# Performance work log

Measured on AMD Instinct MI355X. Metric: run time of the kernel, lower is better.

## Reference

```python
import jax, jax.numpy as jnp
import numpy as np

B, T, C, H = 2, 2048, 1024, 16
HD = C // H  # head dim = 64


def setup_inputs() -> dict:
    key = jax.random.key(0)
    ks = jax.random.split(key, 5)
    s = 0.02
    return {
        "x": jax.random.normal(ks[0], (B, T, C), dtype=jnp.float32),
        "w_attn": jax.random.normal(ks[1], (C, 3 * C), dtype=jnp.float32) * s,
        "b_attn": jnp.zeros((3 * C,), dtype=jnp.float32),
        "w_proj": jax.random.normal(ks[2], (C, C), dtype=jnp.float32) * s,
        "b_proj": jnp.zeros((C,), dtype=jnp.float32),
    }


def reference(x, w_attn, b_attn, w_proj, b_proj):
    Bc, Tc, Cc = x.shape
    qkv = x @ w_attn + b_attn                      # [B,T,3C]
    q, k, v = jnp.split(qkv, 3, axis=2)            # each [B,T,C]
    # [B,T,C] -> [B,H,T,HD]
    def heads(t):
        return t.reshape(Bc, Tc, H, HD).transpose(0, 2, 1, 3)
    q, k, v = heads(q), heads(k), heads(v)
    scale = 1.0 / jnp.sqrt(jnp.asarray(HD, dtype=x.dtype))
    att = jnp.einsum("bhqd,bhkd->bhqk", q, k) * scale   # [B,H,T,T]
    causal = jnp.tril(jnp.ones((Tc, Tc), dtype=bool))
    att = jnp.where(causal, att, jnp.asarray(-jnp.inf, dtype=att.dtype))
    att = jax.nn.softmax(att, axis=-1)
    y = jnp.einsum("bhqk,bhkd->bhqd", att, v)            # [B,H,T,HD]
    y = y.transpose(0, 2, 1, 3).reshape(Bc, Tc, Cc)      # [B,T,C]
    return y @ w_proj + b_proj
```

## Files before the change

### kernel.cpp

```cpp
#include <hip/hip_runtime.h>
#include <stdint.h>


typedef short bf16x8 __attribute__((ext_vector_type(8)));
typedef float f32x4 __attribute__((ext_vector_type(4)));

__device__ inline unsigned short f2bf(float f) {
  union { float f; uint32_t u; } v; v.f = f;
  uint32_t u = v.u;
  u += 0x7FFFu + ((u >> 16) & 1u);
  return (unsigned short)(u >> 16);
}

__device__ inline unsigned pkbf(float a, float b) {
  unsigned r;
  asm("v_cvt_pk_bf16_f32 %0, %1, %2" : "=v"(r) : "v"(a), "v"(b));
  return r;
}

__device__ inline float exp2_fast(float x) {
#if __has_builtin(__builtin_amdgcn_exp2f)
  return __builtin_amdgcn_exp2f(x);
#else
  float r; asm("v_exp_f32 %0, %1" : "=v"(r) : "v"(x)); return r;
#endif
}

__device__ inline void load_lds16(const unsigned short* g, unsigned short* l) {
  __builtin_amdgcn_global_load_lds(
      (const __attribute__((address_space(1))) unsigned int*)(const void*)g,
      (__attribute__((address_space(3))) unsigned int*)(void*)l, 16, 0, 0);
}

__global__ __launch_bounds__(256) void cast_bf16_kernel(
    const float* __restrict__ in, unsigned short* __restrict__ out, int n4) {
  int i = blockIdx.x * 256 + threadIdx.x;
  if (i >= n4) return;
  float4 f = reinterpret_cast<const float4*>(in)[i];
  ushort4 o;
  o.x = f2bf(f.x); o.y = f2bf(f.y); o.z = f2bf(f.z); o.w = f2bf(f.w);
  reinterpret_cast<ushort4*>(out)[i] = o;
}

__global__ void transpose_cast_kernel(
    const float* __restrict__ in, unsigned short* __restrict__ out, int R, int Cn) {
  __shared__ float tile[32][33];
  int bx = blockIdx.x * 32, by = blockIdx.y * 32;
  int tx = threadIdx.x, ty = threadIdx.y;
  #pragma unroll
  for (int i = 0; i < 32; i += 8)
    tile[ty + i][tx] = in[(size_t)(by + ty + i) * Cn + bx + tx];
  __syncthreads();
  #pragma unroll
  for (int i = 0; i < 32; i += 8)
    out[(size_t)(bx + ty + i) * R + by + tx] = f2bf(tile[tx][ty + i]);
}

__global__ __launch_bounds__(256) void gemm_bt_kernel(
    const unsigned short* __restrict__ A,
    const unsigned short* __restrict__ Bt,
    const float* __restrict__ bias,
    void* __restrict__ outp,
    unsigned short* __restrict__ vtp,
    int M, int N, int K, int mode) {
  __shared__ unsigned short As[3][128 * 32];
  __shared__ unsigned short Bs[3][128 * 32];
  const int t = threadIdx.x;
  const int wave = t >> 6, lane = t & 63;
  const int L = lane & 15, quad = lane >> 4;
  const int wm = (wave >> 1) * 64, wn = (wave & 1) * 64;
  const int m0 = blockIdx.y * 128, n0 = blockIdx.x * 128;

  const int drow = lane >> 2;
  const int dch  = (lane & 3) ^ ((drow >> 1) & 3);
  const int foff = ((quad ^ ((L >> 1) & 3)) * 8);

  const unsigned short* Ab = A  + (size_t)(m0 + wave * 32 + drow) * K + dch * 8;
  const unsigned short* Bb = Bt + (size_t)(n0 + wave * 32 + drow) * K + dch * 8;

  f32x4 acc[4][4] = {};
  const int NK = K >> 5;

  #pragma unroll
  for (int j = 0; j < 2; ++j) {
    int r0 = wave * 32 + j * 16;
    load_lds16(Ab + (size_t)j * 16 * K, &As[0][r0 * 32]);
    load_lds16(Bb + (size_t)j * 16 * K, &Bs[0][r0 * 32]);
  }

  int buf = 0;
  for (int kt = 0; kt < NK; ++kt) {
    const int nkt = (kt + 1 < NK) ? kt + 1 : kt;
    const int nbuf = (buf == 2) ? 0 : buf + 1;
    #pragma unroll
    for (int j = 0; j < 2; ++j) {
      int r0 = wave * 32 + j * 16;
      load_lds16(Ab + (size_t)j * 16 * K + nkt * 32, &As[nbuf][r0 * 32]);
      load_lds16(Bb + (size_t)j * 16 * K + nkt * 32, &Bs[nbuf][r0 * 32]);
    }
    asm volatile("" ::: "memory");
    __builtin_amdgcn_s_waitcnt(0x0F74);
    __builtin_amdgcn_s_barrier();
    asm volatile("" ::: "memory");

    bf16x8 af[4], bf[4];
    #pragma unroll
    for (int mt = 0; mt < 4; ++mt)
      af[mt] = *reinterpret_cast<const bf16x8*>(&As[buf][(wm + mt * 16 + L) * 32 + foff]);
    #pragma unroll
    for (int nt = 0; nt < 4; ++nt)
      bf[nt] = *reinterpret_cast<const bf16x8*>(&Bs[buf][(wn + nt * 16 + L) * 32 + foff]);
    __builtin_amdgcn_s_setprio(1);
    #pragma unroll
    for (int mt = 0; mt < 4; ++mt)
      #pragma unroll
      for (int nt = 0; nt < 4; ++nt)
        acc[mt][nt] = __builtin_amdgcn_mfma_f32_16x16x32_bf16(af[mt], bf[nt], acc[mt][nt], 0, 0, 0);
    __builtin_amdgcn_s_setprio(0);
    buf = nbuf;
  }
  __builtin_amdgcn_s_waitcnt(0x0F70);

  if (mode == 0) {
    float* out = (float*)outp;
    #pragma unroll
    for (int mt = 0; mt < 4; ++mt)
      #pragma unroll
      for (int nt = 0; nt < 4; ++nt) {
        int col = n0 + wn + nt * 16 + L;
        float b = bias[col];
        #pragma unroll
        for (int r = 0; r < 4; ++r) {
          int row = m0 + wm + mt * 16 + quad * 4 + r;
          out[(size_t)row * N + col] = acc[mt][nt][r] + b;
        }
      }
  } else {
    unsigned short* qkv = (unsigned short*)outp;
    #pragma unroll
    for (int mt = 0; mt < 4; ++mt)
      #pragma unroll
      for (int nt = 0; nt < 4; ++nt) {
        int col = n0 + wn + nt * 16 + L;
        int sel = col >> 10, cc = col & 1023;
        int h = cc >> 6, d = cc & 63;
        float b = bias[col];
        float sc = (sel == 0) ? 0.18033688011112042f : 1.0f;
        #pragma unroll
        for (int r = 0; r < 4; ++r) {
          int row = m0 + wm + mt * 16 + quad * 4 + r;
          int bb = row >> 11, tt = row & 2047;
          float val = (acc[mt][nt][r] + b) * sc;
          if (sel == 2) {
            vtp[((size_t)(bb * 16 + h) * 64 + d) * 2048 + tt] = f2bf(val);
          } else {
            qkv[(((size_t)sel * 32 + (size_t)(bb * 16 + h)) * 2048 + tt) * 64 + d] = f2bf(val);
          }
        }
      }
  }
}

__global__ __launch_bounds__(256) void attn_kernel(
    const unsigned short* __restrict__ qkv,
    const unsigned short* __restrict__ vt,
    unsigned short* __restrict__ y) {
  __shared__ unsigned short Ks[3][64 * 64];
  __shared__ unsigned short Vs[3][64 * 64];
  __shared__ unsigned short Ps[4][32][72];

  const int t = threadIdx.x;
  const int wave = t >> 6, lane = t & 63;
  const int L = lane & 15, quad = lane >> 4;
  const int b = blockIdx.x;
  const int bh = (b & 7) * 4 + ((b >> 3) & 3);
  const int pi = b >> 5;
  const int tA = pi, tB = 31 - pi;
  const int rowA0 = tA * 64 + wave * 16;
  const int rowB0 = tB * 64 + wave * 16;
  const int ntiles = tB + 1;

  const unsigned short* qb  = qkv + ((size_t)bh * 2048) * 64;
  const unsigned short* kb  = qkv + ((size_t)(32 + bh) * 2048) * 64;
  const unsigned short* vtb = vt + (size_t)bh * 64 * 2048;

  const int drow = lane >> 3;
  const int dch  = (lane & 7) ^ drow;
  const int fo0 = ((quad ^ (L & 7)) * 8);
  const int fo1 = (((quad + 4) ^ (L & 7)) * 8);

  bf16x8 qfA[2], qfB[2];
  #pragma unroll
  for (int h = 0; h < 2; ++h) {
    qfA[h] = *reinterpret_cast<const bf16x8*>(qb + (size_t)(rowA0 + L) * 64 + h * 32 + quad * 8);
    qfB[h] = *reinterpret_cast<const bf16x8*>(qb + (size_t)(rowB0 + L) * 64 + h * 32 + quad * 8);
  }

  f32x4 oA[4] = {}, oB[4] = {};
  float rsA = 0.f, rsB = 0.f;

  {
    #pragma unroll
    for (int j = 0; j < 2; ++j) {
      int r0 = wave * 16 + j * 8;
      load_lds16(kb  + (size_t)(0 + r0 + drow) * 64 + dch * 8, &Ks[0][r0 * 64]);
      load_lds16(vtb + (size_t)(r0 + drow) * 2048 + 0 + dch * 8, &Vs[0][r0 * 64]);
    }
  }

  int buf = 0;
  for (int kt = 0; kt < ntiles; ++kt) {
    const int nkt = (kt + 1 < ntiles) ? kt + 1 : ntiles - 1;
    const int nbuf = (buf == 2) ? 0 : buf + 1;
    {
      const int kg = nkt * 64;
      #pragma unroll
      for (int j = 0; j < 2; ++j) {
        int r0 = wave * 16 + j * 8;
        load_lds16(kb  + (size_t)(kg + r0 + drow) * 64 + dch * 8, &Ks[nbuf][r0 * 64]);
        load_lds16(vtb + (size_t)(r0 + drow) * 2048 + kg + dch * 8, &Vs[nbuf][r0 * 64]);
      }
    }
    asm volatile("" ::: "memory");
    __builtin_amdgcn_s_waitcnt(0x0F74);
    __builtin_amdgcn_s_barrier();
    asm volatile("" ::: "memory");

    const bool actA = (kt <= tA);

    bf16x8 kf[4][2];
    #pragma unroll
    for (int nt = 0; nt < 4; ++nt) {
      kf[nt][0] = *reinterpret_cast<const bf16x8*>(&Ks[buf][(nt * 16 + L) * 64 + fo0]);
      kf[nt][1] = *reinterpret_cast<const bf16x8*>(&Ks[buf][(nt * 16 + L) * 64 + fo1]);
    }

    f32x4 sB[4] = {};
    __builtin_amdgcn_s_setprio(1);
    #pragma unroll
    for (int nt = 0; nt < 4; ++nt) {
      sB[nt] = __builtin_amdgcn_mfma_f32_16x16x32_bf16(kf[nt][0], qfB[0], sB[nt], 0, 0, 0);
      sB[nt] = __builtin_amdgcn_mfma_f32_16x16x32_bf16(kf[nt][1], qfB[1], sB[nt], 0, 0, 0);
    }
    __builtin_amdgcn_s_setprio(0);
    if (kt == tB) {
      #pragma unroll
      for (int nt = 0; nt < 4; ++nt) {
        int key0 = kt * 64 + nt * 16 + quad * 4;
        int qr = rowB0 + L;
        #pragma unroll
        for (int r = 0; r < 4; ++r)
          if (key0 + r > qr) sB[nt][r] = -3.0e38f;
      }
    }
    #pragma unroll
    for (int nt = 0; nt < 4; ++nt) {
      float p0 = exp2_fast(sB[nt][0]), p1 = exp2_fast(sB[nt][1]);
      float p2 = exp2_fast(sB[nt][2]), p3 = exp2_fast(sB[nt][3]);
      rsB += (p0 + p1) + (p2 + p3);
      uint2 pk;
      pk.x = pkbf(p0, p1);
      pk.y = pkbf(p2, p3);
      *reinterpret_cast<uint2*>(&Ps[wave][16 + L][nt * 16 + quad * 4]) = pk;
    }

    if (actA) {
      f32x4 sA[4] = {};
      __builtin_amdgcn_s_setprio(1);
      #pragma unroll
      for (int nt = 0; nt < 4; ++nt) {
        sA[nt] = __builtin_amdgcn_mfma_f32_16x16x32_bf16(kf[nt][0], qfA[0], sA[nt], 0, 0, 0);
        sA[nt] = __builtin_amdgcn_mfma_f32_16x16x32_bf16(kf[nt][1], qfA[1], sA[nt], 0, 0, 0);
      }
      __builtin_amdgcn_s_setprio(0);
      if (kt == tA) {
        #pragma unroll
        for (int nt = 0; nt < 4; ++nt) {
          int key0 = kt * 64 + nt * 16 + quad * 4;
          int qr = rowA0 + L;
          #pragma unroll
          for (int r = 0; r < 4; ++r)
            if (key0 + r > qr) sA[nt][r] = -3.0e38f;
        }
      }
      #pragma unroll
      for (int nt = 0; nt < 4; ++nt) {
        float p0 = exp2_fast(sA[nt][0]), p1 = exp2_fast(sA[nt][1]);
        float p2 = exp2_fast(sA[nt][2]), p3 = exp2_fast(sA[nt][3]);
        rsA += (p0 + p1) + (p2 + p3);
        uint2 pk;
        pk.x = pkbf(p0, p1);
        pk.y = pkbf(p2, p3);
        *reinterpret_cast<uint2*>(&Ps[wave][L][nt * 16 + quad * 4]) = pk;
      }
    }

    bf16x8 vf[4][2];
    #pragma unroll
    for (int nt = 0; nt < 4; ++nt) {
      vf[nt][0] = *reinterpret_cast<const bf16x8*>(&Vs[buf][(nt * 16 + L) * 64 + fo0]);
      vf[nt][1] = *reinterpret_cast<const bf16x8*>(&Vs[buf][(nt * 16 + L) * 64 + fo1]);
    }
    bf16x8 pb0 = *reinterpret_cast<const bf16x8*>(&Ps[wave][16 + L][quad * 8]);
    bf16x8 pb1 = *reinterpret_cast<const bf16x8*>(&Ps[wave][16 + L][32 + quad * 8]);
    __builtin_amdgcn_s_setprio(1);
    #pragma unroll
    for (int nt = 0; nt < 4; ++nt) {
      oB[nt] = __builtin_amdgcn_mfma_f32_16x16x32_bf16(pb0, vf[nt][0], oB[nt], 0, 0, 0);
      oB[nt] = __builtin_amdgcn_mfma_f32_16x16x32_bf16(pb1, vf[nt][1], oB[nt], 0, 0, 0);
    }
    __builtin_amdgcn_s_setprio(0);
    if (actA) {
      bf16x8 pa0 = *reinterpret_cast<const bf16x8*>(&Ps[wave][L][quad * 8]);
      bf16x8 pa1 = *reinterpret_cast<const bf16x8*>(&Ps[wave][L][32 + quad * 8]);
      __builtin_amdgcn_s_setprio(1);
      #pragma unroll
      for (int nt = 0; nt < 4; ++nt) {
        oA[nt] = __builtin_amdgcn_mfma_f32_16x16x32_bf16(pa0, vf[nt][0], oA[nt], 0, 0, 0);
        oA[nt] = __builtin_amdgcn_mfma_f32_16x16x32_bf16(pa1, vf[nt][1], oA[nt], 0, 0, 0);
      }
      __builtin_amdgcn_s_setprio(0);
    }
    buf = nbuf;
  }

  float a = rsA; a += __shfl_xor(a, 16, 64); a += __shfl_xor(a, 32, 64);
  float b2 = rsB; b2 += __shfl_xor(b2, 16, 64); b2 += __shfl_xor(b2, 32, 64);
  float invA[4], invB[4];
  #pragma unroll
  for (int r = 0; r < 4; ++r) {
    invA[r] = 1.0f / __shfl(a, quad * 4 + r, 64);
    invB[r] = 1.0f / __shfl(b2, quad * 4 + r, 64);
  }
  const int bb = bh >> 4, hh = bh & 15;
  #pragma unroll
  for (int nt = 0; nt < 4; ++nt)
    #pragma unroll
    for (int r = 0; r < 4; ++r) {
      int rA = rowA0 + quad * 4 + r;
      int rB = rowB0 + quad * 4 + r;
      int col = hh * 64 + nt * 16 + L;
      y[((size_t)bb * 2048 + rA) * 1024 + col] = f2bf(oA[nt][r] * invA[r]);
      y[((size_t)bb * 2048 + rB) * 1024 + col] = f2bf(oB[nt][r] * invB[r]);
    }
  __builtin_amdgcn_s_waitcnt(0);
}

extern "C" void kernel_launch(void* const* d_in, const int* in_sizes, int n_in,
                              void* d_out, int out_size, void* d_ws, size_t ws_size,
                              hipStream_t stream) {
  const float* x      = (const float*)d_in[0];
  const float* w_attn = (const float*)d_in[1];
  const float* b_attn = (const float*)d_in[2];
  const float* w_proj = (const float*)d_in[3];
  const float* b_proj = (const float*)d_in[4];
  float* out = (float*)d_out;

  unsigned short* ws = (unsigned short*)d_ws;
  unsigned short* xb     = ws;
  unsigned short* wattnT = xb + 4194304;
  unsigned short* wprojT = wattnT + 3145728;
  unsigned short* qkv    = wprojT + 1048576;
  unsigned short* yb     = qkv + 12582912;
  unsigned short* vt     = yb + 4194304;

  cast_bf16_kernel<<<4096, 256, 0, stream>>>(x, xb, 1048576);
  transpose_cast_kernel<<<dim3(96, 32), dim3(32, 8), 0, stream>>>(w_attn, wattnT, 1024, 3072);
  transpose_cast_kernel<<<dim3(32, 32), dim3(32, 8), 0, stream>>>(w_proj, wprojT, 1024, 1024);

  gemm_bt_kernel<<<dim3(24, 32), 256, 0, stream>>>(xb, wattnT, b_attn, qkv, vt, 4096, 3072, 1024, 1);
  attn_kernel<<<dim3(512), 256, 0, stream>>>(qkv, vt, yb);
  gemm_bt_kernel<<<dim3(8, 32), 256, 0, stream>>>(yb, wprojT, b_proj, out, nullptr, 4096, 1024, 1024, 0);
}
```

Measured before the change: 183.9 us.

## Template GEMM tile size, use 64x64 tiles for projection, switch to double buffering

Templates the bf16 GEMM on block tile sizes and launches the output projection with 64x64 tiles, giving 1024 blocks instead of 256 to fill the CUs better. The LDS pipeline also changes from a triple buffer with loads issued before the wait to a double buffer where the next tile's load is issued after the barrier. This shrinks LDS use and may raise occupancy. In exchange each tile stage has less load latency hidden behind the MFMAs, and the smaller tiles reuse data less.

```diff
diff --git a/kernel.cpp b/kernel.cpp
--- a/kernel.cpp
+++ b/kernel.cpp
@@ -56,6 +56,7 @@
     out[(size_t)(bx + ty + i) * R + by + tx] = f2bf(tile[tx][ty + i]);
 }
 
+template<int BM, int BN>
 __global__ __launch_bounds__(256) void gemm_bt_kernel(
     const unsigned short* __restrict__ A,
     const unsigned short* __restrict__ Bt,
@@ -63,70 +64,75 @@
     void* __restrict__ outp,
     unsigned short* __restrict__ vtp,
     int M, int N, int K, int mode) {
-  __shared__ unsigned short As[3][128 * 32];
-  __shared__ unsigned short Bs[3][128 * 32];
+  constexpr int MT = BM / 32, NT = BN / 32;
+  constexpr int RPWA = BM / 4, RPWB = BN / 4;
+  constexpr int NJA = RPWA / 16, NJB = RPWB / 16;
+  __shared__ unsigned short As[2][BM * 32];
+  __shared__ unsigned short Bs[2][BN * 32];
   const int t = threadIdx.x;
   const int wave = t >> 6, lane = t & 63;
   const int L = lane & 15, quad = lane >> 4;
-  const int wm = (wave >> 1) * 64, wn = (wave & 1) * 64;
-  const int m0 = blockIdx.y * 128, n0 = blockIdx.x * 128;
+  const int wm = (wave >> 1) * (BM / 2), wn = (wave & 1) * (BN / 2);
+  const int m0 = blockIdx.y * BM, n0 = blockIdx.x * BN;
 
   const int drow = lane >> 2;
   const int dch  = (lane & 3) ^ ((drow >> 1) & 3);
   const int foff = ((quad ^ ((L >> 1) & 3)) * 8);
 
-  const unsigned short* Ab = A  + (size_t)(m0 + wave * 32 + drow) * K + dch * 8;
-  const unsigned short* Bb = Bt + (size_t)(n0 + wave * 32 + drow) * K + dch * 8;
-
-  f32x4 acc[4][4] = {};
+  const unsigned short* Ab = A  + (size_t)(m0 + wave * RPWA + drow) * K + dch * 8;
+  const unsigned short* Bb = Bt + (size_t)(n0 + wave * RPWB + drow) * K + dch * 8;
+
+  f32x4 acc[MT][NT] = {};
   const int NK = K >> 5;
 
   #pragma unroll
-  for (int j = 0; j < 2; ++j) {
-    int r0 = wave * 32 + j * 16;
-    load_lds16(Ab + (size_t)j * 16 * K, &As[0][r0 * 32]);
-    load_lds16(Bb + (size_t)j * 16 * K, &Bs[0][r0 * 32]);
-  }
+  for (int j = 0; j < NJA; ++j)
+    load_lds16(Ab + (size_t)j * 16 * K, &As[0][(wave * RPWA + j * 16) * 32]);
+  #pragma unroll
+  for (int j = 0; j < NJB; ++j)
+    load_lds16(Bb + (size_t)j * 16 * K, &Bs[0][(wave * RPWB + j * 16) * 32]);
 
   int buf = 0;
   for (int kt = 0; kt < NK; ++kt) {
-    const int nkt = (kt + 1 < NK) ? kt + 1 : kt;
-    const int nbuf = (buf == 2) ? 0 : buf + 1;
-    #pragma unroll
-    for (int j = 0; j < 2; ++j) {
-      int r0 = wave * 32 + j * 16;
-      load_lds16(Ab + (size_t)j * 16 * K + nkt * 32, &As[nbuf][r0 * 32]);
-      load_lds16(Bb + (size_t)j * 16 * K + nkt * 32, &Bs[nbuf][r0 * 32]);
-    }
     asm volatile("" ::: "memory");
-    __builtin_amdgcn_s_waitcnt(0x0F74);
+    __builtin_amdgcn_s_waitcnt(0x0F70);
     __builtin_amdgcn_s_barrier();
     asm volatile("" ::: "memory");
 
-    bf16x8 af[4], bf[4];
-    #pragma unroll
-    for (int mt = 0; mt < 4; ++mt)
+    if (kt + 1 < NK) {
+      #pragma unroll
+      for (int j = 0; j < NJA; ++j)
+        load_lds16(Ab + (size_t)j * 16 * K + (kt + 1) * 32,
+                   &As[buf ^ 1][(wave * RPWA + j * 16) * 32]);
+      #pragma unroll
+      for (int j = 0; j < NJB; ++j)
+        load_lds16(Bb + (size_t)j * 16 * K + (kt + 1) * 32,
+                   &Bs[buf ^ 1][(wave * RPWB + j * 16) * 32]);
+    }
+
+    bf16x8 af[MT], bf[NT];
+    #pragma unroll
+    for (int mt = 0; mt < MT; ++mt)
       af[mt] = *reinterpret_cast<const bf16x8*>(&As[buf][(wm + mt * 16 + L) * 32 + foff]);
     #pragma unroll
-    for (int nt = 0; nt < 4; ++nt)
+    for (int nt = 0; nt < NT; ++nt)
       bf[nt] = *reinterpret_cast<const bf16x8*>(&Bs[buf][(wn + nt * 16 + L) * 32 + foff]);
     __builtin_amdgcn_s_setprio(1);
     #pragma unroll
-    for (int mt = 0; mt < 4; ++mt)
-      #pragma unroll
-      for (int nt = 0; nt < 4; ++nt)
+    for (int mt = 0; mt < MT; ++mt)
+      #pragma unroll
+      for (int nt = 0; nt < NT; ++nt)
         acc[mt][nt] = __builtin_amdgcn_mfma_f32_16x16x32_bf16(af[mt], bf[nt], acc[mt][nt], 0, 0, 0);
     __builtin_amdgcn_s_setprio(0);
-    buf = nbuf;
-  }
-  __builtin_amdgcn_s_waitcnt(0x0F70);
+    buf ^= 1;
+  }
 
   if (mode == 0) {
     float* out = (float*)outp;
     #pragma unroll
-    for (int mt = 0; mt < 4; ++mt)
-      #pragma unroll
-      for (int nt = 0; nt < 4; ++nt) {
+    for (int mt = 0; mt < MT; ++mt)
+      #pragma unroll
+      for (int nt = 0; nt < NT; ++nt) {
         int col = n0 + wn + nt * 16 + L;
         float b = bias[col];
         #pragma unroll
@@ -138,9 +144,9 @@
   } else {
     unsigned short* qkv = (unsigned short*)outp;
     #pragma unroll
-    for (int mt = 0; mt < 4; ++mt)
-      #pragma unroll
-      for (int nt = 0; nt < 4; ++nt) {
+    for (int mt = 0; mt < MT; ++mt)
+      #pragma unroll
+      for (int nt = 0; nt < NT; ++nt) {
         int col = n0 + wn + nt * 16 + L;
         int sel = col >> 10, cc = col & 1023;
         int h = cc >> 6, d = cc & 63;
@@ -368,7 +374,7 @@
   transpose_cast_kernel<<<dim3(96, 32), dim3(32, 8), 0, stream>>>(w_attn, wattnT, 1024, 3072);
   transpose_cast_kernel<<<dim3(32, 32), dim3(32, 8), 0, stream>>>(w_proj, wprojT, 1024, 1024);
 
-  gemm_bt_kernel<<<dim3(24, 32), 256, 0, stream>>>(xb, wattnT, b_attn, qkv, vt, 4096, 3072, 1024, 1);
+  gemm_bt_kernel<128, 128><<<dim3(24, 32), 256, 0, stream>>>(xb, wattnT, b_attn, qkv, vt, 4096, 3072, 1024, 1);
   attn_kernel<<<dim3(512), 256, 0, stream>>>(qkv, vt, yb);
-  gemm_bt_kernel<<<dim3(8, 32), 256, 0, stream>>>(yb, wprojT, b_proj, out, nullptr, 4096, 1024, 1024, 0);
-}
+  gemm_bt_kernel<64, 64><<<dim3(16, 64), 256, 0, stream>>>(yb, wprojT, b_proj, out, nullptr, 4096, 1024, 1024, 0);
+}
```

Result: no change. 181.1 us (-1.5%).
